# Optimization experiments

Hardware: AMD Instinct MI355X
Metric: run time of the kernel (lower is better)

Reference implementation:

```python
import jax, jax.numpy as jnp
import numpy as np

D_MODEL = 1024
NUM_HEADS = 16
D_K = D_MODEL // NUM_HEADS
SCALE = float(np.sqrt(D_K))


def setup_inputs() -> dict:
    key = jax.random.key(0)
    ks = jax.random.split(key, 11)
    B, S, D = 2, 2048, D_MODEL
    def lin(kw):
        # xavier-uniform-ish weight, zero bias (matches torch init style)
        lim = float(np.sqrt(6.0 / (D + D)))
        return jax.random.uniform(kw, (D, D), jnp.float32, -lim, lim)
    return {
        "q": jax.random.normal(ks[0], (B, S, D), jnp.float32),
        "k": jax.random.normal(ks[1], (B, S, D), jnp.float32),
        "v": jax.random.normal(ks[2], (B, S, D), jnp.float32),
        "Wq": lin(ks[3]), "bq": jnp.zeros((D,), jnp.float32),
        "Wk": lin(ks[4]), "bk": jnp.zeros((D,), jnp.float32),
        "Wv": lin(ks[5]), "bv": jnp.zeros((D,), jnp.float32),
        "Wo": lin(ks[6]), "bo": jnp.zeros((D,), jnp.float32),
    }


def _split_heads(x):
    B, S, _ = x.shape
    return x.reshape(B, S, NUM_HEADS, D_K).transpose(0, 2, 1, 3)  # (B,H,S,dk)


def reference(q, k, v, Wq, bq, Wk, bk, Wv, bv, Wo, bo):
    # torch nn.Linear: y = x @ W.T + b
    Q = _split_heads(q @ Wq.T + bq)
    K = _split_heads(k @ Wk.T + bk)
    V = _split_heads(v @ Wv.T + bv)
    scores = jnp.einsum("bhqd,bhkd->bhqk", Q, K) / SCALE
    # numerically-stable softmax with detached max (as in the torch code)
    m = jax.lax.stop_gradient(jnp.max(scores, axis=-1, keepdims=True))
    exp_scores = jnp.exp(scores - m)
    attn = exp_scores / (jnp.sum(exp_scores, axis=-1, keepdims=True) + 1e-9)
    out = jnp.einsum("bhqk,bhkd->bhqd", attn, V)  # (B,H,S,dk)
    B, H, S, dk = out.shape
    out = out.transpose(0, 2, 1, 3).reshape(B, S, H * dk)
    return out @ Wo.T + bo
```

## Files before the change

### kernel.cpp

```cpp
#include <hip/hip_runtime.h>


#define D_MODEL 1024
#define NHEADS  16
#define DKH     64
#define SEQ     2048
#define BATCH   2
#define MTOT    (BATCH * SEQ)
#define XE      ((long)MTOT * D_MODEL)
#define WE      ((long)D_MODEL * D_MODEL)
#define QSCALE  0.18033688011112042f

typedef __attribute__((ext_vector_type(8))) short short8v;
typedef __attribute__((ext_vector_type(4))) short short4v;
typedef __attribute__((ext_vector_type(4))) float f32x4;

typedef __attribute__((address_space(1))) void as1_void;
typedef __attribute__((address_space(3))) void as3_void;

__device__ __forceinline__ void gload16(const void* g, void* l) {
    __builtin_amdgcn_global_load_lds((const as1_void*)g, (as3_void*)l, 16, 0, 0);
}

__device__ __forceinline__ unsigned short f2bf(float x) {
    unsigned int u = __float_as_uint(x);
    u += 0x7FFFu + ((u >> 16) & 1u);
    return (unsigned short)(u >> 16);
}

__device__ __forceinline__ float fexp2(float x) {
    return __builtin_amdgcn_exp2f(x);
}

__device__ __forceinline__ unsigned int cvt_pk_bf16(float lo, float hi) {
    unsigned int r;
    asm("v_cvt_pk_bf16_f32 %0, %1, %2" : "=v"(r) : "v"(lo), "v"(hi));
    return r;
}

__device__ __forceinline__ int swz_u(int row, int col) {
    int byte = (col << 1) ^ ((row & 7) << 4);
    return (row << 6) + (byte >> 1);
}

__device__ __forceinline__ int swz_v(int d, int kv) {
    int slot = (d & 6) | ((d >> 3) & 1);
    int byte = (kv << 1) ^ (slot << 4);
    return (d << 6) + (byte >> 1);
}

struct ConvArgs {
    const float*    src[7];
    unsigned short* dst[7];
    int             n4[7];
};

__global__ __launch_bounds__(256) void convert_kernel(ConvArgs a) {
    int z = blockIdx.y;
    const float4*   s = (const float4*)a.src[z];
    unsigned short* d = a.dst[z];
    int n = a.n4[z];
    for (int i = blockIdx.x * blockDim.x + threadIdx.x; i < n;
         i += gridDim.x * blockDim.x) {
        float4 v = s[i];
        ushort4 o;
        o.x = f2bf(v.x); o.y = f2bf(v.y); o.z = f2bf(v.z); o.w = f2bf(v.w);
        *(ushort4*)(d + 4L * i) = o;
    }
}

__device__ __forceinline__ void stv(float* p, float v)          { *p = v; }
__device__ __forceinline__ void stv(unsigned short* p, float v) { *p = f2bf(v); }

template <typename OutT>
__device__ __forceinline__ void gemm_core(const unsigned short* __restrict__ A,
                                          const unsigned short* __restrict__ Bm,
                                          const float* __restrict__ bias,
                                          OutT* __restrict__ C,
                                          int K, int N, float scale,
                                          long m0, long n0) {
    __shared__ unsigned short As[128 * 32];
    __shared__ unsigned short Bs[128 * 32];

    const int t    = threadIdx.x;
    const int lane = t & 63;
    const int w    = t >> 6;
    const int wm   = w >> 1, wn = w & 1;
    const int l15  = lane & 15, g = lane >> 4;

    f32x4 acc[4][4] = {};

    const int idx0 = t, idx1 = t + 256;
    const int r0 = idx0 >> 2, c0 = (idx0 & 3) * 8;
    const int r1 = idx1 >> 2, c1 = (idx1 & 3) * 8;
    const unsigned short* pa0 = A  + (m0 + r0) * K + c0;
    const unsigned short* pa1 = A  + (m0 + r1) * K + c1;
    const unsigned short* pb0 = Bm + (n0 + r0) * K + c0;
    const unsigned short* pb1 = Bm + (n0 + r1) * K + c1;

    for (int k0 = 0; k0 < K; k0 += 32) {
        gload16(pa0 + k0, &As[idx0 * 8]);
        gload16(pa1 + k0, &As[idx1 * 8]);
        gload16(pb0 + k0, &Bs[idx0 * 8]);
        gload16(pb1 + k0, &Bs[idx1 * 8]);
        __syncthreads();

        short8v af[4], bf_[4];
#pragma unroll
        for (int mf = 0; mf < 4; ++mf)
            af[mf] = *(const short8v*)&As[(wm * 64 + mf * 16 + l15) * 32 + g * 8];
#pragma unroll
        for (int nf = 0; nf < 4; ++nf)
            bf_[nf] = *(const short8v*)&Bs[(wn * 64 + nf * 16 + l15) * 32 + g * 8];
#pragma unroll
        for (int mf = 0; mf < 4; ++mf)
#pragma unroll
            for (int nf = 0; nf < 4; ++nf)
                acc[mf][nf] = __builtin_amdgcn_mfma_f32_16x16x32_bf16(
                    af[mf], bf_[nf], acc[mf][nf], 0, 0, 0);
        __syncthreads();
    }

    float bvv[4];
#pragma unroll
    for (int nf = 0; nf < 4; ++nf)
        bvv[nf] = bias[n0 + wn * 64 + nf * 16 + l15];

#pragma unroll
    for (int mf = 0; mf < 4; ++mf)
#pragma unroll
        for (int nf = 0; nf < 4; ++nf)
#pragma unroll
            for (int r = 0; r < 4; ++r) {
                long row = m0 + wm * 64 + mf * 16 + g * 4 + r;
                long col = n0 + wn * 64 + nf * 16 + l15;
                float v = (acc[mf][nf][r] + bvv[nf]) * scale;
                stv(C + row * (long)N + col, v);
            }
}

__global__ __launch_bounds__(256) void proj_kernel(
    const unsigned short* __restrict__ xb, const unsigned short* __restrict__ wb,
    const float* __restrict__ bq, const float* __restrict__ bk,
    const float* __restrict__ bv, unsigned short* __restrict__ qkv) {
    const int bid = blockIdx.x;
    const int xcd = bid & 7;
    const int k   = bid >> 3;
    const int ty  = (xcd << 2) | (k & 3);
    const int tx  = (k >> 2) & 7;
    const int z   = k >> 5;
    const float* bias = (z == 0) ? bq : (z == 1) ? bk : bv;
    float scale = (z == 0) ? QSCALE : 1.0f;
    gemm_core<unsigned short>(xb + (long)z * XE, wb + (long)z * WE, bias,
                              qkv + (long)z * XE, D_MODEL, D_MODEL, scale,
                              (long)ty * 128, (long)tx * 128);
}

__global__ __launch_bounds__(256) void out_kernel(
    const unsigned short* __restrict__ ob, const unsigned short* __restrict__ wo,
    const float* __restrict__ bo, float* __restrict__ out) {
    const int bid = blockIdx.x;
    const int xcd = bid & 7;
    const int k   = bid >> 3;
    const int ty  = (xcd << 2) | (k & 3);
    const int tx  = k >> 2;
    gemm_core<float>(ob, wo, bo, out, D_MODEL, D_MODEL, 1.0f,
                     (long)ty * 128, (long)tx * 128);
}

#define KVB 4096

__global__ __launch_bounds__(512) void attn_kernel(
    const unsigned short* __restrict__ Qb, const unsigned short* __restrict__ Kb,
    const unsigned short* __restrict__ Vb, unsigned short* __restrict__ Ob) {
    __shared__ alignas(16) unsigned short Ks[2 * KVB];
    __shared__ alignas(16) unsigned short Vt[2 * KVB];
    __shared__ alignas(16) unsigned short Ps[8][16 * 64];
    __shared__ alignas(16) float corrS[8][16];

    const int t = threadIdx.x, lane = t & 63, w = t >> 6;
    const int l15 = lane & 15, g = lane >> 4;
    const int bid = blockIdx.x;
    const int xcd = bid & 7;
    const int kk2 = bid >> 3;
    const int bh  = (xcd << 2) | (kk2 & 3);
    const int qb  = kk2 >> 2;
    const long headoff = (long)(bh >> 4) * SEQ * D_MODEL + (long)(bh & 15) * DKH;
    const int q0w = qb * 128 + w * 16;

    short8v qf[2];
#pragma unroll
    for (int ks = 0; ks < 2; ++ks)
        qf[ks] = *(const short8v*)(Qb + headoff +
            (long)(q0w + l15) * D_MODEL + ks * 32 + g * 8);

    short8v onesv;
#pragma unroll
    for (int j = 0; j < 8; ++j) onesv[j] = (short)0x3F80;

    f32x4 o[4] = {};
    f32x4 ol = {};
    float mrun = -3.0e38f;

    const int vd0  = (t & 31) * 2;
    const int vkv0 = (t >> 5) * 4;
    const int kr0 = t >> 3, ks0 = t & 7;

    unsigned int va[4];

#define ISSUE_V(kt)                                                        \
    _Pragma("unroll")                                                      \
    for (int j = 0; j < 4; ++j)                                            \
        va[j] = *(const unsigned int*)(Vb + headoff +                      \
            (long)((kt) + vkv0 + j) * D_MODEL + vd0);

#define ISSUE_K(kt, off)                                                   \
    gload16(Kb + headoff + (long)((kt) + kr0) * D_MODEL +                  \
                ((ks0 ^ (kr0 & 7)) << 3), &Ks[(off) + t * 8]);

#define WRITE_V(off)                                                       \
    {                                                                      \
        short4v ra, rb;                                                    \
        _Pragma("unroll")                                                  \
        for (int j = 0; j < 4; ++j) {                                      \
            ra[j] = (short)(va[j] & 0xffffu);                              \
            rb[j] = (short)(va[j] >> 16);                                  \
        }                                                                  \
        *(short4v*)&Vt[(off) + swz_v(vd0,     vkv0)] = ra;                 \
        *(short4v*)&Vt[(off) + swz_v(vd0 + 1, vkv0)] = rb;                 \
    }

    asm volatile("s_waitcnt vmcnt(0)" ::: "memory");
    ISSUE_V(0);
    ISSUE_K(0, 0);
    WRITE_V(0);
    int cur = 0;

    for (int it = 0; it < SEQ / 64; ++it) {
        const int nxt = cur ^ 1;
        const int ktn = (((it + 1) & (SEQ / 64 - 1))) * 64;
        ISSUE_V(ktn);
        ISSUE_K(ktn, nxt * KVB);
        asm volatile("s_waitcnt vmcnt(5)" ::: "memory");
        asm volatile("s_waitcnt lgkmcnt(0)" ::: "memory");
        __builtin_amdgcn_sched_barrier(0);
        __builtin_amdgcn_s_barrier();
        __builtin_amdgcn_sched_barrier(0);

        const int kO = cur * KVB;

        f32x4 st[4] = {};
        __builtin_amdgcn_s_setprio(1);
#pragma unroll
        for (int ks = 0; ks < 2; ++ks)
#pragma unroll
            for (int mf = 0; mf < 4; ++mf) {
                short8v kf = *(const short8v*)&Ks[kO + swz_u(mf * 16 + l15, ks * 32 + g * 8)];
                st[mf] = __builtin_amdgcn_mfma_f32_16x16x32_bf16(
                    kf, qf[ks], st[mf], 0, 0, 0);
            }
        __builtin_amdgcn_s_setprio(0);

        float vmax = st[0][0];
#pragma unroll
        for (int mf = 0; mf < 4; ++mf)
#pragma unroll
            for (int r = 0; r < 4; ++r)
                vmax = fmaxf(vmax, st[mf][r]);
        vmax = fmaxf(vmax, __shfl_xor(vmax, 16));
        vmax = fmaxf(vmax, __shfl_xor(vmax, 32));

        const bool grow = __any(vmax > mrun + 8.0f);
        if (grow) {
            float mnew = fmaxf(mrun, vmax);
            float corr = fexp2(mrun - mnew);
            mrun = mnew;
            if (g == 0) corrS[w][l15] = corr;
        }

#pragma unroll
        for (int mf = 0; mf < 4; ++mf)
#pragma unroll
            for (int r = 0; r < 4; ++r)
                st[mf][r] = fexp2(st[mf][r] - mrun);

        unsigned short* Pw = Ps[w];
#pragma unroll
        for (int mf = 0; mf < 4; ++mf) {
            uint2 pk;
            pk.x = cvt_pk_bf16(st[mf][0], st[mf][1]);
            pk.y = cvt_pk_bf16(st[mf][2], st[mf][3]);
            *(uint2*)&Pw[swz_u(l15, mf * 16 + g * 4)] = pk;
        }

        if (grow) {
            float4 cv = *(const float4*)&corrS[w][g * 4];
#pragma unroll
            for (int nd = 0; nd < 4; ++nd)
#pragma unroll
                for (int r = 0; r < 4; ++r)
                    o[nd][r] *= cv[r];
#pragma unroll
            for (int r = 0; r < 4; ++r) ol[r] *= cv[r];
        }

        __builtin_amdgcn_s_setprio(1);
#pragma unroll
        for (int ks2 = 0; ks2 < 2; ++ks2) {
            short8v pf = *(const short8v*)&Pw[swz_u(l15, ks2 * 32 + g * 8)];
            ol = __builtin_amdgcn_mfma_f32_16x16x32_bf16(
                pf, onesv, ol, 0, 0, 0);
#pragma unroll
            for (int nd = 0; nd < 4; ++nd) {
                short8v vf = *(const short8v*)&Vt[kO + swz_v(nd * 16 + l15, ks2 * 32 + g * 8)];
                o[nd] = __builtin_amdgcn_mfma_f32_16x16x32_bf16(
                    pf, vf, o[nd], 0, 0, 0);
            }
        }
        __builtin_amdgcn_s_setprio(0);

        WRITE_V(nxt * KVB);
        cur = nxt;
    }

#pragma unroll
    for (int r = 0; r < 4; ++r) {
        float inv = 1.f / (ol[r] + 1e-9f);
        long rowoff = headoff + (long)(q0w + g * 4 + r) * D_MODEL;
#pragma unroll
        for (int nd = 0; nd < 4; ++nd)
            Ob[rowoff + nd * 16 + l15] = f2bf(o[nd][r] * inv);
    }
#undef ISSUE_V
#undef ISSUE_K
#undef WRITE_V
}

extern "C" void kernel_launch(void* const* d_in, const int* in_sizes, int n_in,
                              void* d_out, int out_size, void* d_ws, size_t ws_size,
                              hipStream_t stream) {
    unsigned short* ws  = (unsigned short*)d_ws;
    unsigned short* xb  = ws;
    unsigned short* wb  = ws + 3L * XE;
    unsigned short* qkv = ws + 3L * XE + 4L * WE;
    unsigned short* ob  = qkv + 3L * XE;

    ConvArgs ca;
    ca.src[0] = (const float*)d_in[0]; ca.dst[0] = xb;           ca.n4[0] = (int)(XE / 4);
    ca.src[1] = (const float*)d_in[1]; ca.dst[1] = xb + XE;      ca.n4[1] = (int)(XE / 4);
    ca.src[2] = (const float*)d_in[2]; ca.dst[2] = xb + 2L * XE; ca.n4[2] = (int)(XE / 4);
    ca.src[3] = (const float*)d_in[3]; ca.dst[3] = wb;           ca.n4[3] = (int)(WE / 4);
    ca.src[4] = (const float*)d_in[5]; ca.dst[4] = wb + WE;      ca.n4[4] = (int)(WE / 4);
    ca.src[5] = (const float*)d_in[7]; ca.dst[5] = wb + 2L * WE; ca.n4[5] = (int)(WE / 4);
    ca.src[6] = (const float*)d_in[9]; ca.dst[6] = wb + 3L * WE; ca.n4[6] = (int)(WE / 4);

    hipLaunchKernelGGL(convert_kernel, dim3(512, 7), dim3(256), 0, stream, ca);

    hipLaunchKernelGGL(proj_kernel, dim3(768), dim3(256), 0, stream,
                       xb, wb, (const float*)d_in[4], (const float*)d_in[6],
                       (const float*)d_in[8], qkv);

    hipLaunchKernelGGL(attn_kernel, dim3(512), dim3(512), 0, stream,
                       qkv, qkv + XE, qkv + 2L * XE, ob);

    hipLaunchKernelGGL(out_kernel, dim3(256), dim3(256), 0, stream,
                       ob, wb + 3L * WE, (const float*)d_in[10], (float*)d_out);
}
```

Before: 133.5 us.

## Rewrite QKV projection GEMM with 256x256 tiles, double-buffered swizzled LDS

The QKV projection kernel now uses 256x256 output tiles with a 64-wide K step and 512 threads. It double-buffers LDS so the next tile's global-to-LDS loads overlap the current MFMA work, XOR-swizzles the LDS layout to avoid bank conflicts, and raises wave priority around MFMA bursts. The grid shrinks from 768 to 192 blocks, which is fewer than the CU count, so occupancy and load balance may suffer in exchange for higher per-block data reuse. The output GEMM is inlined unchanged.

```diff
diff --git a/kernel.cpp b/kernel.cpp
--- a/kernel.cpp
+++ b/kernel.cpp
@@ -69,16 +69,131 @@
     }
 }
 
-__device__ __forceinline__ void stv(float* p, float v)          { *p = v; }
-__device__ __forceinline__ void stv(unsigned short* p, float v) { *p = f2bf(v); }
-
-template <typename OutT>
-__device__ __forceinline__ void gemm_core(const unsigned short* __restrict__ A,
-                                          const unsigned short* __restrict__ Bm,
-                                          const float* __restrict__ bias,
-                                          OutT* __restrict__ C,
-                                          int K, int N, float scale,
-                                          long m0, long n0) {
+#define PBM 256
+#define PBK 64
+#define PTILE (PBM * PBK)
+
+__global__ __launch_bounds__(512) void proj_kernel(
+    const unsigned short* __restrict__ xb, const unsigned short* __restrict__ wb,
+    const float* __restrict__ bq, const float* __restrict__ bk,
+    const float* __restrict__ bv, unsigned short* __restrict__ qkv) {
+    __shared__ unsigned short As[2 * PTILE];
+    __shared__ unsigned short Bs[2 * PTILE];
+
+    const int t    = threadIdx.x;
+    const int lane = t & 63;
+    const int w    = t >> 6;
+    const int wm   = w >> 2, wn = w & 3;
+    const int l15  = lane & 15, g = lane >> 4;
+
+    const int bid = blockIdx.x;
+    const int xcd = bid & 7;
+    const int k   = bid >> 3;
+    const int ty  = (xcd << 1) | (k & 1);
+    const int tx  = (k >> 1) & 3;
+    const int z   = k >> 3;
+    const float* bias = (z == 0) ? bq : (z == 1) ? bk : bv;
+    const float scale = (z == 0) ? QSCALE : 1.0f;
+
+    const unsigned short* A  = xb + (long)z * XE;
+    const unsigned short* Bm = wb + (long)z * WE;
+    unsigned short*       C  = qkv + (long)z * XE;
+    const long m0 = (long)ty * PBM;
+    const long n0 = (long)tx * PBM;
+    const int  K  = D_MODEL;
+
+    f32x4 acc[8][4] = {};
+
+    int srow[4], scol[4];
+#pragma unroll
+    for (int c = 0; c < 4; ++c) {
+        int idx = t + c * 512;
+        srow[c] = idx >> 3;
+        scol[c] = ((idx & 7) ^ (srow[c] & 7)) * 8;
+    }
+
+#define PSTAGE(k0, buf)                                                    \
+    _Pragma("unroll")                                                      \
+    for (int c = 0; c < 4; ++c) {                                          \
+        int idx = t + c * 512;                                             \
+        gload16(A  + (m0 + srow[c]) * K + (k0) + scol[c],                  \
+                &As[(buf) * PTILE + idx * 8]);                             \
+        gload16(Bm + (n0 + srow[c]) * K + (k0) + scol[c],                  \
+                &Bs[(buf) * PTILE + idx * 8]);                             \
+    }
+
+    PSTAGE(0, 0);
+    int cur = 0;
+
+    for (int it = 0; it < K / PBK; ++it) {
+        const int nxt = cur ^ 1;
+        const int kn  = ((it + 1) * PBK) & (K - 1);
+        PSTAGE(kn, nxt);
+        asm volatile("s_waitcnt vmcnt(8)" ::: "memory");
+        asm volatile("s_waitcnt lgkmcnt(0)" ::: "memory");
+        __builtin_amdgcn_sched_barrier(0);
+        __builtin_amdgcn_s_barrier();
+        __builtin_amdgcn_sched_barrier(0);
+
+        const unsigned short* Ab = &As[cur * PTILE];
+        const unsigned short* Bb = &Bs[cur * PTILE];
+
+#pragma unroll
+        for (int kk = 0; kk < 2; ++kk) {
+            short8v bf_[4];
+#pragma unroll
+            for (int nf = 0; nf < 4; ++nf) {
+                int r = wn * 64 + nf * 16 + l15;
+                bf_[nf] = *(const short8v*)&Bb[r * 64 + (((kk * 4 + g) ^ (r & 7)) * 8)];
+            }
+#pragma unroll
+            for (int mh = 0; mh < 2; ++mh) {
+                short8v af_[4];
+#pragma unroll
+                for (int i = 0; i < 4; ++i) {
+                    int r = wm * 128 + (mh * 4 + i) * 16 + l15;
+                    af_[i] = *(const short8v*)&Ab[r * 64 + (((kk * 4 + g) ^ (r & 7)) * 8)];
+                }
+                __builtin_amdgcn_s_setprio(1);
+#pragma unroll
+                for (int i = 0; i < 4; ++i)
+#pragma unroll
+                    for (int nf = 0; nf < 4; ++nf)
+                        acc[mh * 4 + i][nf] = __builtin_amdgcn_mfma_f32_16x16x32_bf16(
+                            af_[i], bf_[nf], acc[mh * 4 + i][nf], 0, 0, 0);
+                __builtin_amdgcn_s_setprio(0);
+            }
+        }
+
+        asm volatile("s_waitcnt lgkmcnt(0)" ::: "memory");
+        __builtin_amdgcn_sched_barrier(0);
+        __builtin_amdgcn_s_barrier();
+        __builtin_amdgcn_sched_barrier(0);
+        cur = nxt;
+    }
+
+    float bvv[4];
+#pragma unroll
+    for (int nf = 0; nf < 4; ++nf)
+        bvv[nf] = bias[n0 + wn * 64 + nf * 16 + l15];
+
+#pragma unroll
+    for (int mf = 0; mf < 8; ++mf)
+#pragma unroll
+        for (int nf = 0; nf < 4; ++nf)
+#pragma unroll
+            for (int r = 0; r < 4; ++r) {
+                long row = m0 + wm * 128 + mf * 16 + g * 4 + r;
+                long col = n0 + wn * 64 + nf * 16 + l15;
+                C[row * (long)D_MODEL + col] =
+                    f2bf((acc[mf][nf][r] + bvv[nf]) * scale);
+            }
+#undef PSTAGE
+}
+
+__global__ __launch_bounds__(256) void out_kernel(
+    const unsigned short* __restrict__ ob, const unsigned short* __restrict__ wo,
+    const float* __restrict__ bo, float* __restrict__ out) {
     __shared__ unsigned short As[128 * 32];
     __shared__ unsigned short Bs[128 * 32];
 
@@ -88,15 +203,22 @@
     const int wm   = w >> 1, wn = w & 1;
     const int l15  = lane & 15, g = lane >> 4;
 
+    const int bid = blockIdx.x;
+    const int xcd = bid & 7;
+    const int k   = bid >> 3;
+    const long m0 = (long)((xcd << 2) | (k & 3)) * 128;
+    const long n0 = (long)(k >> 2) * 128;
+    const int  K  = D_MODEL, N = D_MODEL;
+
     f32x4 acc[4][4] = {};
 
     const int idx0 = t, idx1 = t + 256;
     const int r0 = idx0 >> 2, c0 = (idx0 & 3) * 8;
     const int r1 = idx1 >> 2, c1 = (idx1 & 3) * 8;
-    const unsigned short* pa0 = A  + (m0 + r0) * K + c0;
-    const unsigned short* pa1 = A  + (m0 + r1) * K + c1;
-    const unsigned short* pb0 = Bm + (n0 + r0) * K + c0;
-    const unsigned short* pb1 = Bm + (n0 + r1) * K + c1;
+    const unsigned short* pa0 = ob + (m0 + r0) * K + c0;
+    const unsigned short* pa1 = ob + (m0 + r1) * K + c1;
+    const unsigned short* pb0 = wo + (n0 + r0) * K + c0;
+    const unsigned short* pb1 = wo + (n0 + r1) * K + c1;
 
     for (int k0 = 0; k0 < K; k0 += 32) {
         gload16(pa0 + k0, &As[idx0 * 8]);
@@ -124,7 +246,7 @@
     float bvv[4];
 #pragma unroll
     for (int nf = 0; nf < 4; ++nf)
-        bvv[nf] = bias[n0 + wn * 64 + nf * 16 + l15];
+        bvv[nf] = bo[n0 + wn * 64 + nf * 16 + l15];
 
 #pragma unroll
     for (int mf = 0; mf < 4; ++mf)
@@ -134,38 +256,8 @@
             for (int r = 0; r < 4; ++r) {
                 long row = m0 + wm * 64 + mf * 16 + g * 4 + r;
                 long col = n0 + wn * 64 + nf * 16 + l15;
-                float v = (acc[mf][nf][r] + bvv[nf]) * scale;
-                stv(C + row * (long)N + col, v);
-            }
-}
-
-__global__ __launch_bounds__(256) void proj_kernel(
-    const unsigned short* __restrict__ xb, const unsigned short* __restrict__ wb,
-    const float* __restrict__ bq, const float* __restrict__ bk,
-    const float* __restrict__ bv, unsigned short* __restrict__ qkv) {
-    const int bid = blockIdx.x;
-    const int xcd = bid & 7;
-    const int k   = bid >> 3;
-    const int ty  = (xcd << 2) | (k & 3);
-    const int tx  = (k >> 2) & 7;
-    const int z   = k >> 5;
-    const float* bias = (z == 0) ? bq : (z == 1) ? bk : bv;
-    float scale = (z == 0) ? QSCALE : 1.0f;
-    gemm_core<unsigned short>(xb + (long)z * XE, wb + (long)z * WE, bias,
-                              qkv + (long)z * XE, D_MODEL, D_MODEL, scale,
-                              (long)ty * 128, (long)tx * 128);
-}
-
-__global__ __launch_bounds__(256) void out_kernel(
-    const unsigned short* __restrict__ ob, const unsigned short* __restrict__ wo,
-    const float* __restrict__ bo, float* __restrict__ out) {
-    const int bid = blockIdx.x;
-    const int xcd = bid & 7;
-    const int k   = bid >> 3;
-    const int ty  = (xcd << 2) | (k & 3);
-    const int tx  = k >> 2;
-    gemm_core<float>(ob, wo, bo, out, D_MODEL, D_MODEL, 1.0f,
-                     (long)ty * 128, (long)tx * 128);
+                out[row * (long)N + col] = acc[mf][nf][r] + bvv[nf];
+            }
 }
 
 #define KVB 4096
@@ -356,7 +448,7 @@
 
     hipLaunchKernelGGL(convert_kernel, dim3(512, 7), dim3(256), 0, stream, ca);
 
-    hipLaunchKernelGGL(proj_kernel, dim3(768), dim3(256), 0, stream,
+    hipLaunchKernelGGL(proj_kernel, dim3(192), dim3(512), 0, stream,
                        xb, wb, (const float*)d_in[4], (const float*)d_in[6],
                        (const float*)d_in[8], qkv);
 
```

Measured after the change: 132.7 us. Within noise of the previous version (-0.6%).
